# Kernel tuning notes

Measured on AMD Instinct MI355X. Metric: run time of the kernel, lower is better.

## Reference

```python
import jax, jax.numpy as jnp
import numpy as np

NTOKENS = 50257
NHID = 1024
NPC = int(np.ceil(np.sqrt(NTOKENS)))            # 225 tokens per class
NCLASSES = int(np.ceil(NTOKENS / NPC))          # 224 classes
BATCH = 1024
INITRANGE = 0.1


def setup_inputs() -> dict:
    key = jax.random.key(0)
    k1, k2, k3, k4 = jax.random.split(key, 4)
    inputs = jax.random.normal(k1, (BATCH, NHID), dtype=jnp.float32)
    labels = jax.random.randint(k2, (BATCH,), 0, NTOKENS, dtype=jnp.int64)
    layer_top_W = jax.random.uniform(k3, (NHID, NCLASSES), minval=-INITRANGE, maxval=INITRANGE, dtype=jnp.float32)
    layer_top_b = jnp.zeros((NCLASSES,), dtype=jnp.float32)
    layer_bottom_W = jax.random.uniform(k4, (NCLASSES, NHID, NPC), minval=-INITRANGE, maxval=INITRANGE, dtype=jnp.float32)
    layer_bottom_b = jnp.zeros((NCLASSES, NPC), dtype=jnp.float32)
    return {
        "inputs": inputs,
        "labels": labels,
        "layer_top_W": layer_top_W,
        "layer_top_b": layer_top_b,
        "layer_bottom_W": layer_bottom_W,
        "layer_bottom_b": layer_bottom_b,
    }


def reference(inputs, labels, layer_top_W, layer_top_b, layer_bottom_W, layer_bottom_b):
    batch_size = inputs.shape[0]
    # decompose label into (class, within-class) position; old-torch `/` on Long == floor div
    pos_top = labels // NPC            # [B]
    pos_bottom = labels % NPC          # [B]

    # top-level class distribution: [B, nclasses]
    top_logits = inputs @ layer_top_W + layer_top_b
    top_probs = jax.nn.softmax(top_logits, axis=1)

    # gather per-sample class weight slices and do batched matvec:
    # layer_bottom_W[pos_top]: [B, nhid, npc]
    bottom_logits = jnp.einsum("bd,bdc->bc", inputs, layer_bottom_W[pos_top]) + layer_bottom_b[pos_top]
    bottom_probs = jax.nn.softmax(bottom_logits, axis=1)

    rows = jnp.arange(batch_size)
    target_probs = top_probs[rows, pos_top] * bottom_probs[rows, pos_bottom]  # [B]
    return target_probs
```

## Files before the change

kernel.cpp:

```cpp
#include <hip/hip_runtime.h>
#include <math.h>

#define NHID 1024
#define NPC  225
#define NCLS 224
#define BATCH 1024
#define N_BOT 352
#define N_TOP (BATCH / 8)

#define WS_PT 0
#define WS_PB 1024

__global__ __launch_bounds__(1024, 4) void k_fused(const float* __restrict__ X,
                                                   const int* __restrict__ labels,
                                                   const float* __restrict__ Wt,
                                                   const float* __restrict__ bt,
                                                   const float* __restrict__ Wb,
                                                   const float* __restrict__ bb,
                                                   float* __restrict__ ws)
{
    __shared__ __align__(16) float sm[14848];
    __shared__ int cnt_[256];
    __shared__ int iscan_[256];
    __shared__ int slot[8];
    __shared__ int wtot[16];
    __shared__ int cls_sh;

    const int tid  = threadIdx.x;
    const int wave = tid >> 6;
    const int lane = tid & 63;
    const int j8   = tid & 7;
    const int t8   = tid >> 3;

    if ((int)blockIdx.x < N_BOT) {
        if (tid < 256) cnt_[tid] = 0;
        __syncthreads();
        const int myc = labels[tid] / NPC;
        atomicAdd(&cnt_[myc], 1);
        __syncthreads();
        if (tid < 256) iscan_[tid] = (tid < NCLS) ? ((cnt_[tid] + 7) >> 3) : 0;
        __syncthreads();
        for (int off = 1; off < 256; off <<= 1) {
            int a = 0;
            if (tid < 256 && tid >= off) a = iscan_[tid - off];
            __syncthreads();
            if (tid < 256) iscan_[tid] += a;
            __syncthreads();
        }
        if ((int)blockIdx.x >= iscan_[255]) return;
        if (tid < NCLS) {
            const int lo = (tid == 0) ? 0 : iscan_[tid - 1];
            if ((int)blockIdx.x >= lo && (int)blockIdx.x < iscan_[tid]) cls_sh = tid;
        }
        __syncthreads();
        const int cls    = cls_sh;
        const int ibase  = (cls == 0) ? 0 : iscan_[cls - 1];
        const int within = (int)blockIdx.x - ibase;
        const int cnt    = cnt_[cls];
        const int nt     = min(8, cnt - 8 * within);

        {
            const bool flag = (myc == cls);
            const unsigned long long m = __ballot(flag);
            if (lane == 0) wtot[wave] = __popcll(m);
            __syncthreads();
            if (flag) {
                int pos = __popcll(m & ((1ull << lane) - 1));
#pragma unroll
                for (int w = 0; w < 16; ++w)
                    if (w < wave) pos += wtot[w];
                const int r = pos - 8 * within;
                if (r >= 0 && r < 8) slot[r] = tid;
            }
            __syncthreads();
        }

        const int sid = (j8 < nt) ? slot[j8] : -1;
        for (int d4 = t8; d4 < 256; d4 += 128) {
            float4 v = make_float4(0.f, 0.f, 0.f, 0.f);
            if (sid >= 0) v = ((const float4*)&X[(size_t)sid * NHID])[d4];
            float* p = &sm[48 * d4 + j8];
            p[0] = v.x; p[12] = v.y; p[24] = v.z; p[36] = v.w;
        }
        __syncthreads();

        float acc[8][4];
#pragma unroll
        for (int j = 0; j < 8; ++j)
#pragma unroll
            for (int k = 0; k < 4; ++k) acc[j][k] = 0.f;

        const int c0 = lane, c1 = lane + 64, c2 = lane + 128, c3 = lane + 192;
        const bool m3 = (c3 < NPC);
        const int d0 = wave * 64;
        const float* Wr = Wb + (size_t)cls * (NHID * NPC) + (size_t)d0 * NPC;

        auto ldrow = [&](int r, float* o) {
            const float* p = Wr + (size_t)r * NPC;
            o[0] = __builtin_nontemporal_load(p + c0);
            o[1] = __builtin_nontemporal_load(p + c1);
            o[2] = __builtin_nontemporal_load(p + c2);
            o[3] = m3 ? __builtin_nontemporal_load(p + c3) : 0.f;
        };
        float wbuf[4][4];
        ldrow(0, wbuf[0]); ldrow(1, wbuf[1]); ldrow(2, wbuf[2]); ldrow(3, wbuf[3]);

#pragma unroll 4
        for (int dd = 0; dd < 64; ++dd) {
            const int slot4 = dd & 3;
            const float cw0 = wbuf[slot4][0], cw1 = wbuf[slot4][1],
                        cw2 = wbuf[slot4][2], cw3 = wbuf[slot4][3];
            ldrow(min(dd + 4, 63), wbuf[slot4]);
            const float4 a = *(const float4*)&sm[(d0 + dd) * 12 + 0];
            const float4 b = *(const float4*)&sm[(d0 + dd) * 12 + 4];
            const float xi[8] = {a.x, a.y, a.z, a.w, b.x, b.y, b.z, b.w};
#pragma unroll
            for (int j = 0; j < 8; ++j) {
                acc[j][0] = fmaf(xi[j], cw0, acc[j][0]);
                acc[j][1] = fmaf(xi[j], cw1, acc[j][1]);
                acc[j][2] = fmaf(xi[j], cw2, acc[j][2]);
                acc[j][3] = fmaf(xi[j], cw3, acc[j][3]);
            }
        }
        __syncthreads();

        float* red = sm;
        if (wave >= 8) {
#pragma unroll
            for (int j = 0; j < 8; ++j)
#pragma unroll
                for (int k = 0; k < 4; ++k) {
                    int c = lane + 64 * k;
                    if (c < NPC) red[((wave - 8) * 8 + j) * 232 + c] = acc[j][k];
                }
        }
        __syncthreads();
        if (wave < 8) {
#pragma unroll
            for (int j = 0; j < 8; ++j)
#pragma unroll
                for (int k = 0; k < 4; ++k) {
                    int c = lane + 64 * k;
                    if (c < NPC) red[(wave * 8 + j) * 232 + c] += acc[j][k];
                }
        }
        __syncthreads();

        if (wave < 8) {
            const int j = wave;
            if (j < nt) {
                const int s = slot[j];
                float v[4];
#pragma unroll
                for (int k = 0; k < 4; ++k) {
                    int c = lane + 64 * k;
                    if (c < NPC) {
                        float t = bb[(size_t)cls * NPC + c];
#pragma unroll
                        for (int g = 0; g < 8; ++g) t += red[(g * 8 + j) * 232 + c];
                        v[k] = t;
                    } else v[k] = -INFINITY;
                }
                float m = fmaxf(fmaxf(v[0], v[1]), fmaxf(v[2], v[3]));
                for (int o = 32; o > 0; o >>= 1) m = fmaxf(m, __shfl_xor(m, o));
                float e = expf(v[0] - m) + expf(v[1] - m) + expf(v[2] - m) + expf(v[3] - m);
                for (int o = 32; o > 0; o >>= 1) e += __shfl_xor(e, o);
                const int pb = labels[s] % NPC;
                if (lane == (pb & 63))
                    ws[WS_PB + s] = expf(v[pb >> 6] - m) / e;
            }
        }
        return;
    }

    const int sbase = ((int)blockIdx.x - N_BOT) * 8;

    for (int d4 = t8; d4 < 256; d4 += 128) {
        const float4 v = ((const float4*)&X[(size_t)(sbase + j8) * NHID])[d4];
        float* p = &sm[48 * d4 + j8];
        p[0] = v.x; p[12] = v.y; p[24] = v.z; p[36] = v.w;
    }
    __syncthreads();

    float acc[8][4];
#pragma unroll
    for (int j = 0; j < 8; ++j)
#pragma unroll
        for (int k = 0; k < 4; ++k) acc[j][k] = 0.f;

    const int c0 = lane, c1 = lane + 64, c2 = lane + 128, c3 = lane + 192;
    const bool m3 = (c3 < NCLS);
    const int d0 = wave * 64;
    const float* Wr = Wt + (size_t)d0 * NCLS;

    auto ldrow = [&](int r, float* o) {
        const float* p = Wr + (size_t)r * NCLS;
        o[0] = p[c0]; o[1] = p[c1]; o[2] = p[c2];
        o[3] = m3 ? p[c3] : 0.f;
    };
    float wbuf[4][4];
    ldrow(0, wbuf[0]); ldrow(1, wbuf[1]); ldrow(2, wbuf[2]); ldrow(3, wbuf[3]);

#pragma unroll 4
    for (int dd = 0; dd < 64; ++dd) {
        const int slot4 = dd & 3;
        const float cw0 = wbuf[slot4][0], cw1 = wbuf[slot4][1],
                    cw2 = wbuf[slot4][2], cw3 = wbuf[slot4][3];
        ldrow(min(dd + 4, 63), wbuf[slot4]);
        const float4 a = *(const float4*)&sm[(d0 + dd) * 12 + 0];
        const float4 b = *(const float4*)&sm[(d0 + dd) * 12 + 4];
        const float xi[8] = {a.x, a.y, a.z, a.w, b.x, b.y, b.z, b.w};
#pragma unroll
        for (int j = 0; j < 8; ++j) {
            acc[j][0] = fmaf(xi[j], cw0, acc[j][0]);
            acc[j][1] = fmaf(xi[j], cw1, acc[j][1]);
            acc[j][2] = fmaf(xi[j], cw2, acc[j][2]);
            acc[j][3] = fmaf(xi[j], cw3, acc[j][3]);
        }
    }
    __syncthreads();

    float* red = sm;
    if (wave >= 8) {
#pragma unroll
        for (int j = 0; j < 8; ++j)
#pragma unroll
            for (int k = 0; k < 4; ++k) {
                int c = lane + 64 * k;
                if (c < NCLS) red[((wave - 8) * 8 + j) * 232 + c] = acc[j][k];
            }
    }
    __syncthreads();
    if (wave < 8) {
#pragma unroll
        for (int j = 0; j < 8; ++j)
#pragma unroll
            for (int k = 0; k < 4; ++k) {
                int c = lane + 64 * k;
                if (c < NCLS) red[(wave * 8 + j) * 232 + c] += acc[j][k];
            }
    }
    __syncthreads();

    if (wave < 8) {
        const int j = wave;
        const int s = sbase + j;
        float v[4];
#pragma unroll
        for (int k = 0; k < 4; ++k) {
            int c = lane + 64 * k;
            if (c < NCLS) {
                float t = bt[c];
#pragma unroll
                for (int g = 0; g < 8; ++g) t += red[(g * 8 + j) * 232 + c];
                v[k] = t;
            } else v[k] = -INFINITY;
        }
        float m = fmaxf(fmaxf(v[0], v[1]), fmaxf(v[2], v[3]));
        for (int o = 32; o > 0; o >>= 1) m = fmaxf(m, __shfl_xor(m, o));
        float e = expf(v[0] - m) + expf(v[1] - m) + expf(v[2] - m) + expf(v[3] - m);
        for (int o = 32; o > 0; o >>= 1) e += __shfl_xor(e, o);
        const int pt = labels[s] / NPC;
        if (lane == (pt & 63))
            ws[WS_PT + s] = expf(v[pt >> 6] - m) / e;
    }
}

__global__ void k_mul(const float* __restrict__ ws, float* __restrict__ out)
{
    const int i = blockIdx.x * 256 + threadIdx.x;
    if (i < BATCH) out[i] = ws[WS_PT + i] * ws[WS_PB + i];
}

extern "C" void kernel_launch(void* const* d_in, const int* in_sizes, int n_in,
                              void* d_out, int out_size, void* d_ws, size_t ws_size,
                              hipStream_t stream)
{
    const float* X      = (const float*)d_in[0];
    const int*   labels = (const int*)  d_in[1];
    const float* Wt     = (const float*)d_in[2];
    const float* bt     = (const float*)d_in[3];
    const float* Wb     = (const float*)d_in[4];
    const float* bb     = (const float*)d_in[5];

    hipLaunchKernelGGL(k_fused, dim3(N_BOT + N_TOP), dim3(1024), 0, stream,
                       X, labels, Wt, bt, Wb, bb, (float*)d_ws);
    hipLaunchKernelGGL(k_mul, dim3(BATCH / 256), dim3(256), 0, stream,
                       (const float*)d_ws, (float*)d_out);
}
```

Measured before the change: 304.1 us.

## Use persistent 256-block grid looping over bottom items, then fold top work in

Replaces the split grid of bottom and top blocks with 256 persistent blocks. Each block loops over the bottom work items, using a binary search over the class prefix scan to find its class, then computes the top softmax for 4 samples. The bottom weight rows are now loaded as contiguous 4-float vector nontemporal loads per lane instead of strided scalar loads, and the reduction uses float4 shared-memory accesses. This is meant to cut block-launch imbalance and improve load efficiency, at the cost of serialized items per block and extra barriers.

Result: slower. 321.2 us (+5.6%).

```diff
diff --git a/kernel.cpp b/kernel.cpp
--- a/kernel.cpp
+++ b/kernel.cpp
@@ -5,8 +5,9 @@
 #define NPC  225
 #define NCLS 224
 #define BATCH 1024
-#define N_BOT 352
-#define N_TOP (BATCH / 8)
+#define NBLK  256
+
+typedef float f4u __attribute__((ext_vector_type(4), aligned(4)));
 
 #define WS_PT 0
 #define WS_PB 1024
@@ -19,53 +20,53 @@
                                                    const float* __restrict__ bb,
                                                    float* __restrict__ ws)
 {
-    __shared__ __align__(16) float sm[14848];
+    __shared__ __align__(16) float sm[15360];
     __shared__ int cnt_[256];
     __shared__ int iscan_[256];
     __shared__ int slot[8];
     __shared__ int wtot[16];
-    __shared__ int cls_sh;
 
     const int tid  = threadIdx.x;
     const int wave = tid >> 6;
     const int lane = tid & 63;
     const int j8   = tid & 7;
     const int t8   = tid >> 3;
-
-    if ((int)blockIdx.x < N_BOT) {
-        if (tid < 256) cnt_[tid] = 0;
-        __syncthreads();
-        const int myc = labels[tid] / NPC;
-        atomicAdd(&cnt_[myc], 1);
-        __syncthreads();
-        if (tid < 256) iscan_[tid] = (tid < NCLS) ? ((cnt_[tid] + 7) >> 3) : 0;
-        __syncthreads();
-        for (int off = 1; off < 256; off <<= 1) {
-            int a = 0;
-            if (tid < 256 && tid >= off) a = iscan_[tid - off];
-            __syncthreads();
-            if (tid < 256) iscan_[tid] += a;
-            __syncthreads();
-        }
-        if ((int)blockIdx.x >= iscan_[255]) return;
-        if (tid < NCLS) {
-            const int lo = (tid == 0) ? 0 : iscan_[tid - 1];
-            if ((int)blockIdx.x >= lo && (int)blockIdx.x < iscan_[tid]) cls_sh = tid;
-        }
-        __syncthreads();
-        const int cls    = cls_sh;
+    const int bid  = blockIdx.x;
+
+    if (tid < 256) cnt_[tid] = 0;
+    __syncthreads();
+    const int myc = labels[tid] / NPC;
+    atomicAdd(&cnt_[myc], 1);
+    __syncthreads();
+    if (tid < 256) iscan_[tid] = (tid < NCLS) ? ((cnt_[tid] + 7) >> 3) : 0;
+    __syncthreads();
+    for (int off = 1; off < 256; off <<= 1) {
+        int a = 0;
+        if (tid < 256 && tid >= off) a = iscan_[tid - off];
+        __syncthreads();
+        if (tid < 256 && tid >= off) iscan_[tid] += a;
+        __syncthreads();
+    }
+    const int nitems = iscan_[255];
+
+    for (int item = bid; item < nitems; item += NBLK) {
+        int lo = 0, hi = NCLS - 1;
+        while (lo < hi) {
+            const int mid = (lo + hi) >> 1;
+            if (iscan_[mid] > item) hi = mid; else lo = mid + 1;
+        }
+        const int cls    = lo;
         const int ibase  = (cls == 0) ? 0 : iscan_[cls - 1];
-        const int within = (int)blockIdx.x - ibase;
-        const int cnt    = cnt_[cls];
-        const int nt     = min(8, cnt - 8 * within);
+        const int within = item - ibase;
+        const int nt     = min(8, cnt_[cls] - 8 * within);
 
         {
             const bool flag = (myc == cls);
-            const unsigned long long m = __ballot(flag);
-            if (lane == 0) wtot[wave] = __popcll(m);
+            const unsigned long long mb = __ballot(flag);
+            if (lane == 0) wtot[wave] = __popcll(mb);
             __syncthreads();
             if (flag) {
-                int pos = __popcll(m & ((1ull << lane) - 1));
+                int pos = __popcll(mb & ((1ull << lane) - 1));
 #pragma unroll
                 for (int w = 0; w < 16; ++w)
                     if (w < wave) pos += wtot[w];
@@ -90,101 +91,105 @@
 #pragma unroll
             for (int k = 0; k < 4; ++k) acc[j][k] = 0.f;
 
-        const int c0 = lane, c1 = lane + 64, c2 = lane + 128, c3 = lane + 192;
-        const bool m3 = (c3 < NPC);
         const int d0 = wave * 64;
         const float* Wr = Wb + (size_t)cls * (NHID * NPC) + (size_t)d0 * NPC;
 
-        auto ldrow = [&](int r, float* o) {
+        f4u wbuf[4];
+        auto ldrow = [&](int r, f4u& o) {
             const float* p = Wr + (size_t)r * NPC;
-            o[0] = __builtin_nontemporal_load(p + c0);
-            o[1] = __builtin_nontemporal_load(p + c1);
-            o[2] = __builtin_nontemporal_load(p + c2);
-            o[3] = m3 ? __builtin_nontemporal_load(p + c3) : 0.f;
+            f4u t = {0.f, 0.f, 0.f, 0.f};
+            if (lane < 56)       t = __builtin_nontemporal_load((const f4u*)(p + 4 * lane));
+            else if (lane == 56) t.x = __builtin_nontemporal_load(p + 224);
+            o = t;
         };
-        float wbuf[4][4];
         ldrow(0, wbuf[0]); ldrow(1, wbuf[1]); ldrow(2, wbuf[2]); ldrow(3, wbuf[3]);
 
 #pragma unroll 4
         for (int dd = 0; dd < 64; ++dd) {
-            const int slot4 = dd & 3;
-            const float cw0 = wbuf[slot4][0], cw1 = wbuf[slot4][1],
-                        cw2 = wbuf[slot4][2], cw3 = wbuf[slot4][3];
-            ldrow(min(dd + 4, 63), wbuf[slot4]);
+            const int sl = dd & 3;
+            const f4u cw = wbuf[sl];
+            ldrow(min(dd + 4, 63), wbuf[sl]);
             const float4 a = *(const float4*)&sm[(d0 + dd) * 12 + 0];
             const float4 b = *(const float4*)&sm[(d0 + dd) * 12 + 4];
             const float xi[8] = {a.x, a.y, a.z, a.w, b.x, b.y, b.z, b.w};
 #pragma unroll
             for (int j = 0; j < 8; ++j) {
-                acc[j][0] = fmaf(xi[j], cw0, acc[j][0]);
-                acc[j][1] = fmaf(xi[j], cw1, acc[j][1]);
-                acc[j][2] = fmaf(xi[j], cw2, acc[j][2]);
-                acc[j][3] = fmaf(xi[j], cw3, acc[j][3]);
+                acc[j][0] = fmaf(xi[j], cw.x, acc[j][0]);
+                acc[j][1] = fmaf(xi[j], cw.y, acc[j][1]);
+                acc[j][2] = fmaf(xi[j], cw.z, acc[j][2]);
+                acc[j][3] = fmaf(xi[j], cw.w, acc[j][3]);
             }
         }
         __syncthreads();
 
         float* red = sm;
-        if (wave >= 8) {
+        if (wave >= 8 && lane <= 56) {
 #pragma unroll
             for (int j = 0; j < 8; ++j)
-#pragma unroll
-                for (int k = 0; k < 4; ++k) {
-                    int c = lane + 64 * k;
-                    if (c < NPC) red[((wave - 8) * 8 + j) * 232 + c] = acc[j][k];
+                *(float4*)&red[((wave - 8) * 8 + j) * 240 + 4 * lane] =
+                    make_float4(acc[j][0], acc[j][1], acc[j][2], acc[j][3]);
+        }
+        __syncthreads();
+        if (wave < 8 && lane <= 56) {
+#pragma unroll
+            for (int j = 0; j < 8; ++j) {
+                float4* q = (float4*)&red[(wave * 8 + j) * 240 + 4 * lane];
+                float4 t = *q;
+                t.x += acc[j][0]; t.y += acc[j][1];
+                t.z += acc[j][2]; t.w += acc[j][3];
+                *q = t;
+            }
+        }
+        __syncthreads();
+
+        if (wave < 8 && wave < nt) {
+            const int j = wave;
+            const int s = slot[j];
+            const int cb = 4 * lane;
+            float v0 = -INFINITY, v1 = -INFINITY, v2 = -INFINITY, v3 = -INFINITY;
+            if (lane <= 56) {
+                float t0 = bb[(size_t)cls * NPC + cb];
+                float t1 = (cb + 1 < NPC) ? bb[(size_t)cls * NPC + cb + 1] : 0.f;
+                float t2 = (cb + 2 < NPC) ? bb[(size_t)cls * NPC + cb + 2] : 0.f;
+                float t3 = (cb + 3 < NPC) ? bb[(size_t)cls * NPC + cb + 3] : 0.f;
+#pragma unroll
+                for (int g = 0; g < 8; ++g) {
+                    const float4 rg = *(const float4*)&red[(g * 8 + j) * 240 + cb];
+                    t0 += rg.x; t1 += rg.y; t2 += rg.z; t3 += rg.w;
                 }
-        }
-        __syncthreads();
-        if (wave < 8) {
-#pragma unroll
-            for (int j = 0; j < 8; ++j)
-#pragma unroll
-                for (int k = 0; k < 4; ++k) {
-                    int c = lane + 64 * k;
-                    if (c < NPC) red[(wave * 8 + j) * 232 + c] += acc[j][k];
-                }
-        }
-        __syncthreads();
-
-        if (wave < 8) {
-            const int j = wave;
-            if (j < nt) {
-                const int s = slot[j];
-                float v[4];
-#pragma unroll
-                for (int k = 0; k < 4; ++k) {
-                    int c = lane + 64 * k;
-                    if (c < NPC) {
-                        float t = bb[(size_t)cls * NPC + c];
-#pragma unroll
-                        for (int g = 0; g < 8; ++g) t += red[(g * 8 + j) * 232 + c];
-                        v[k] = t;
-                    } else v[k] = -INFINITY;
-                }
-                float m = fmaxf(fmaxf(v[0], v[1]), fmaxf(v[2], v[3]));
-                for (int o = 32; o > 0; o >>= 1) m = fmaxf(m, __shfl_xor(m, o));
-                float e = expf(v[0] - m) + expf(v[1] - m) + expf(v[2] - m) + expf(v[3] - m);
-                for (int o = 32; o > 0; o >>= 1) e += __shfl_xor(e, o);
-                const int pb = labels[s] % NPC;
-                if (lane == (pb & 63))
-                    ws[WS_PB + s] = expf(v[pb >> 6] - m) / e;
-            }
-        }
-        return;
-    }
-
-    const int sbase = ((int)blockIdx.x - N_BOT) * 8;
-
-    for (int d4 = t8; d4 < 256; d4 += 128) {
-        const float4 v = ((const float4*)&X[(size_t)(sbase + j8) * NHID])[d4];
-        float* p = &sm[48 * d4 + j8];
-        p[0] = v.x; p[12] = v.y; p[24] = v.z; p[36] = v.w;
-    }
-    __syncthreads();
-
-    float acc[8][4];
-#pragma unroll
-    for (int j = 0; j < 8; ++j)
+                v0 = t0;
+                v1 = (cb + 1 < NPC) ? t1 : -INFINITY;
+                v2 = (cb + 2 < NPC) ? t2 : -INFINITY;
+                v3 = (cb + 3 < NPC) ? t3 : -INFINITY;
+            }
+            float m = fmaxf(fmaxf(v0, v1), fmaxf(v2, v3));
+            for (int o = 32; o > 0; o >>= 1) m = fmaxf(m, __shfl_xor(m, o));
+            float e = expf(v0 - m) + expf(v1 - m) + expf(v2 - m) + expf(v3 - m);
+            for (int o = 32; o > 0; o >>= 1) e += __shfl_xor(e, o);
+            const int pb = labels[s] % NPC;
+            if (lane == (pb >> 2)) {
+                const int kk = pb & 3;
+                const float vs = kk == 0 ? v0 : kk == 1 ? v1 : kk == 2 ? v2 : v3;
+                ws[WS_PB + s] = expf(vs - m) / e;
+            }
+        }
+        __syncthreads();
+    }
+
+    __syncthreads();
+    const int sbase = bid * 4;
+    {
+        const int j4 = tid & 3;
+        const int d4 = tid >> 2;
+        const float4 xv = ((const float4*)&X[(size_t)(sbase + j4) * NHID])[d4];
+        float* p = &sm[16 * d4 + j4];
+        p[0] = xv.x; p[4] = xv.y; p[8] = xv.z; p[12] = xv.w;
+    }
+    __syncthreads();
+
+    float acc[4][4];
+#pragma unroll
+    for (int j = 0; j < 4; ++j)
 #pragma unroll
         for (int k = 0; k < 4; ++k) acc[j][k] = 0.f;
 
@@ -193,25 +198,24 @@
     const int d0 = wave * 64;
     const float* Wr = Wt + (size_t)d0 * NCLS;
 
-    auto ldrow = [&](int r, float* o) {
+    auto ldrowT = [&](int r, float* o) {
         const float* p = Wr + (size_t)r * NCLS;
         o[0] = p[c0]; o[1] = p[c1]; o[2] = p[c2];
         o[3] = m3 ? p[c3] : 0.f;
     };
-    float wbuf[4][4];
-    ldrow(0, wbuf[0]); ldrow(1, wbuf[1]); ldrow(2, wbuf[2]); ldrow(3, wbuf[3]);
+    float wb[4][4];
+    ldrowT(0, wb[0]); ldrowT(1, wb[1]); ldrowT(2, wb[2]); ldrowT(3, wb[3]);
 
 #pragma unroll 4
     for (int dd = 0; dd < 64; ++dd) {
-        const int slot4 = dd & 3;
-        const float cw0 = wbuf[slot4][0], cw1 = wbuf[slot4][1],
-                    cw2 = wbuf[slot4][2], cw3 = wbuf[slot4][3];
-        ldrow(min(dd + 4, 63), wbuf[slot4]);
-        const float4 a = *(const float4*)&sm[(d0 + dd) * 12 + 0];
-        const float4 b = *(const float4*)&sm[(d0 + dd) * 12 + 4];
-        const float xi[8] = {a.x, a.y, a.z, a.w, b.x, b.y, b.z, b.w};
-#pragma unroll
-        for (int j = 0; j < 8; ++j) {
+        const int sl = dd & 3;
+        const float cw0 = wb[sl][0], cw1 = wb[sl][1],
+                    cw2 = wb[sl][2], cw3 = wb[sl][3];
+        ldrowT(min(dd + 4, 63), wb[sl]);
+        const float4 a = *(const float4*)&sm[4 * (d0 + dd)];
+        const float xi[4] = {a.x, a.y, a.z, a.w};
+#pragma unroll
+        for (int j = 0; j < 4; ++j) {
             acc[j][0] = fmaf(xi[j], cw0, acc[j][0]);
             acc[j][1] = fmaf(xi[j], cw1, acc[j][1]);
             acc[j][2] = fmaf(xi[j], cw2, acc[j][2]);
@@ -223,46 +227,53 @@
     float* red = sm;
     if (wave >= 8) {
 #pragma unroll
-        for (int j = 0; j < 8; ++j)
+        for (int j = 0; j < 4; ++j)
 #pragma unroll
             for (int k = 0; k < 4; ++k) {
-                int c = lane + 64 * k;
-                if (c < NCLS) red[((wave - 8) * 8 + j) * 232 + c] = acc[j][k];
+                const int c = lane + 64 * k;
+                if (c < NCLS) red[((wave - 8) * 4 + j) * 232 + c] = acc[j][k];
             }
     }
     __syncthreads();
     if (wave < 8) {
 #pragma unroll
-        for (int j = 0; j < 8; ++j)
+        for (int j = 0; j < 4; ++j)
 #pragma unroll
             for (int k = 0; k < 4; ++k) {
-                int c = lane + 64 * k;
-                if (c < NCLS) red[(wave * 8 + j) * 232 + c] += acc[j][k];
-            }
-    }
-    __syncthreads();
-
-    if (wave < 8) {
+                const int c = lane + 64 * k;
+                if (c < NCLS) red[(wave * 4 + j) * 232 + c] += acc[j][k];
+            }
+    }
+    __syncthreads();
+
+    if (wave < 4) {
         const int j = wave;
         const int s = sbase + j;
-        float v[4];
-#pragma unroll
-        for (int k = 0; k < 4; ++k) {
-            int c = lane + 64 * k;
-            if (c < NCLS) {
-                float t = bt[c];
-#pragma unroll
-                for (int g = 0; g < 8; ++g) t += red[(g * 8 + j) * 232 + c];
-                v[k] = t;
-            } else v[k] = -INFINITY;
-        }
-        float m = fmaxf(fmaxf(v[0], v[1]), fmaxf(v[2], v[3]));
+        float v0, v1, v2, v3;
+        {
+            float vv[4];
+#pragma unroll
+            for (int k = 0; k < 4; ++k) {
+                const int c = lane + 64 * k;
+                if (c < NCLS) {
+                    float t = bt[c];
+#pragma unroll
+                    for (int g = 0; g < 8; ++g) t += red[(g * 4 + j) * 232 + c];
+                    vv[k] = t;
+                } else vv[k] = -INFINITY;
+            }
+            v0 = vv[0]; v1 = vv[1]; v2 = vv[2]; v3 = vv[3];
+        }
+        float m = fmaxf(fmaxf(v0, v1), fmaxf(v2, v3));
         for (int o = 32; o > 0; o >>= 1) m = fmaxf(m, __shfl_xor(m, o));
-        float e = expf(v[0] - m) + expf(v[1] - m) + expf(v[2] - m) + expf(v[3] - m);
+        float e = expf(v0 - m) + expf(v1 - m) + expf(v2 - m) + expf(v3 - m);
         for (int o = 32; o > 0; o >>= 1) e += __shfl_xor(e, o);
         const int pt = labels[s] / NPC;
-        if (lane == (pt & 63))
-            ws[WS_PT + s] = expf(v[pt >> 6] - m) / e;
+        if (lane == (pt & 63)) {
+            const int kk = pt >> 6;
+            const float vs = kk == 0 ? v0 : kk == 1 ? v1 : kk == 2 ? v2 : v3;
+            ws[WS_PT + s] = expf(vs - m) / e;
+        }
     }
 }
 
@@ -283,7 +294,7 @@
     const float* Wb     = (const float*)d_in[4];
     const float* bb     = (const float*)d_in[5];
 
-    hipLaunchKernelGGL(k_fused, dim3(N_BOT + N_TOP), dim3(1024), 0, stream,
+    hipLaunchKernelGGL(k_fused, dim3(NBLK), dim3(1024), 0, stream,
                        X, labels, Wt, bt, Wb, bb, (float*)d_ws);
     hipLaunchKernelGGL(k_mul, dim3(BATCH / 256), dim3(256), 0, stream,
                        (const float*)d_ws, (float*)d_out);
```
